# Optimization experiments

Hardware: AMD Instinct MI355X
Metric: run time of the kernel (lower is better)

Reference implementation:

```python
import jax, jax.numpy as jnp
import numpy as np

# Hard-coded module constants (from source)
E = 384      # EMBEDDING_SIZE
H = 6        # HEAD_NO
HS = 64      # HEAD_SIZE = E // H
T_CTX = 256  # CONTEXT_LENGTH
L = 6        # LAYER_NO
V = 50257    # vocab_size (init kwarg)
B = 16       # batch
T = 256      # sequence length (== context length)


def setup_inputs() -> dict:
    key = jax.random.key(0)
    ks = jax.random.split(key, 12)
    p = lambda k, shape: jax.random.normal(k, shape, dtype=jnp.float32) * 0.02
    return {
        "idx": jax.random.randint(ks[0], (B, T), 0, V),
        "tok_emb": p(ks[1], (V, E)),
        "pos_emb": p(ks[2], (T_CTX, E)),
        # per-layer stacked params; per-head q/k/v weights concatenated into [E, E]
        "Wq": p(ks[3], (L, E, E)),
        "Wk": p(ks[4], (L, E, E)),
        "Wv": p(ks[5], (L, E, E)),
        "Wo": p(ks[6], (L, E, E)),
        "bo": jnp.zeros((L, E), jnp.float32),
        "ln1_g": jnp.ones((L, E), jnp.float32),
        "ln1_b": jnp.zeros((L, E), jnp.float32),
        "ln2_g": jnp.ones((L, E), jnp.float32),
        "ln2_b": jnp.zeros((L, E), jnp.float32),
        "Wm": p(ks[7], (L, E, E)),  # MLP: single Linear(E,E) + ReLU
        "bm": jnp.zeros((L, E), jnp.float32),
        "lnf_g": jnp.ones((E,), jnp.float32),
        "lnf_b": jnp.zeros((E,), jnp.float32),
        "Wlm": p(ks[8], (E, V)),
        "blm": jnp.zeros((V,), jnp.float32),
    }


def _layernorm(x, g, b):
    mu = jnp.mean(x, axis=-1, keepdims=True)
    var = jnp.var(x, axis=-1, keepdims=True)  # biased, matches torch LayerNorm
    return (x - mu) / jnp.sqrt(var + 1e-5) * g + b


def _forward(idx, tok_emb, pos_emb, Wq, Wk, Wv, Wo, bo, ln1_g, ln1_b,
             ln2_g, ln2_b, Wm, bm, lnf_g, lnf_b, Wlm, blm):
    Bb, Tt = idx.shape
    x = tok_emb[idx] + pos_emb[:Tt]                        # [B,T,E]
    causal = jnp.tril(jnp.ones((Tt, Tt), bool))            # tril buffer
    scale = 1.0 / jnp.sqrt(jnp.float32(HS))

    def block(x, lp):
        wq, wk, wv, wo, bo_, g1, b1, g2, b2, wm, bm_ = lp
        h = _layernorm(x, g1, b1)
        q = (h @ wq).reshape(Bb, Tt, H, HS)
        k = (h @ wk).reshape(Bb, Tt, H, HS)
        v = (h @ wv).reshape(Bb, Tt, H, HS)
        s = jnp.einsum('bqhd,bkhd->bhqk', q, k)
        # source: masked_fill(-inf) then divide by sqrt(HS); -inf stays -inf
        s = jnp.where(causal, s, -jnp.inf) * scale
        a = jax.nn.softmax(s, axis=-1)                     # dropout: eval mode (no-op)
        o = jnp.einsum('bhqk,bkhd->bqhd', a, v).reshape(Bb, Tt, E)
        x = x + (o @ wo + bo_)                             # proj + residual
        h2 = _layernorm(x, g2, b2)
        x = x + jax.nn.relu(h2 @ wm + bm_)                 # MLP is Linear+ReLU only
        return x, None

    x, _ = jax.lax.scan(block, x, (Wq, Wk, Wv, Wo, bo, ln1_g, ln1_b,
                                   ln2_g, ln2_b, Wm, bm))
    x = _layernorm(x, lnf_g, lnf_b)
    return x @ Wlm + blm                                   # [B,T,V] logits


def reference(idx, tok_emb, pos_emb, Wq, Wk, Wv, Wo, bo, ln1_g, ln1_b,
              ln2_g, ln2_b, Wm, bm, lnf_g, lnf_b, Wlm, blm):
    return _forward(idx, tok_emb, pos_emb, Wq, Wk, Wv, Wo, bo, ln1_g, ln1_b,
                    ln2_g, ln2_b, Wm, bm, lnf_g, lnf_b, Wlm, blm)
```

## Files before the change

kernel.cpp:

```cpp
#include <hip/hip_runtime.h>
#include <hip/hip_bf16.h>
#include <math.h>

#define E_DIM 384
#define N_HEAD 6
#define HEAD_SZ 64
#define SEQ 256
#define BATCH 16
#define NTOK 4096
#define NLAYER 6
#define VOCAB 50257
#define VPAD 50304
#define QKV_N 1152
#define NBH 96

typedef __attribute__((ext_vector_type(8))) short bf16x8;
typedef __attribute__((ext_vector_type(4))) float f32x4;

__device__ __forceinline__ void gload16(const void* g, void* l) {
    __builtin_amdgcn_global_load_lds((const __attribute__((address_space(1))) char*)g,
                                     (__attribute__((address_space(3))) char*)l, 16, 0, 0);
}

__global__ void embed_kernel(const int* __restrict__ idx,
                             const float* __restrict__ tok,
                             const float* __restrict__ pos,
                             float* __restrict__ x) {
    int i = blockIdx.x * blockDim.x + threadIdx.x;
    if (i >= NTOK * E_DIM) return;
    int m = i / E_DIM, e = i - m * E_DIM;
    int t = m & (SEQ - 1);
    x[i] = tok[(size_t)idx[m] * E_DIM + e] + pos[t * E_DIM + e];
}

__global__ __launch_bounds__(256) void ln_kernel(const float* __restrict__ x,
                                                 const float* __restrict__ g,
                                                 const float* __restrict__ b,
                                                 __hip_bfloat16* __restrict__ h) {
    int lane = threadIdx.x & 63;
    int wave = threadIdx.x >> 6;
    int row  = blockIdx.x * 4 + wave;
    const float* xr = x + (size_t)row * E_DIM;
    float v[6];
    float s = 0.f;
#pragma unroll
    for (int c = 0; c < 6; ++c) { v[c] = xr[lane + 64 * c]; s += v[c]; }
#pragma unroll
    for (int off = 32; off > 0; off >>= 1) s += __shfl_xor(s, off);
    float mu = s * (1.0f / E_DIM);
    float s2 = 0.f;
#pragma unroll
    for (int c = 0; c < 6; ++c) { float d = v[c] - mu; s2 += d * d; }
#pragma unroll
    for (int off = 32; off > 0; off >>= 1) s2 += __shfl_xor(s2, off);
    float rstd = rsqrtf(s2 * (1.0f / E_DIM) + 1e-5f);
    __hip_bfloat16* hr = h + (size_t)row * E_DIM;
#pragma unroll
    for (int c = 0; c < 6; ++c) {
        int e = lane + 64 * c;
        hr[e] = __float2bfloat16((v[c] - mu) * rstd * g[e] + b[e]);
    }
}

__device__ __forceinline__ void tconv_tile(const float* __restrict__ src,
                                           __hip_bfloat16* __restrict__ dst,
                                           int K, int N, int n0, int k0) {
    __shared__ float tbuf[64][65];
    int c = threadIdx.x & 63, r4 = threadIdx.x >> 6;
#pragma unroll
    for (int i = 0; i < 16; ++i) {
        int r = r4 * 16 + i;
        float v = 0.f;
        if (n0 + c < N) v = src[(size_t)(k0 + r) * N + n0 + c];
        tbuf[r][c] = v;
    }
    __syncthreads();
#pragma unroll
    for (int i = 0; i < 16; ++i) {
        int rn = r4 * 16 + i;
        dst[(size_t)(n0 + rn) * K + k0 + c] = __float2bfloat16(tbuf[c][rn]);
    }
}

__global__ __launch_bounds__(256) void tconv_layers(const float* __restrict__ Wq,
                                                    const float* __restrict__ Wk,
                                                    const float* __restrict__ Wv,
                                                    const float* __restrict__ Wo,
                                                    const float* __restrict__ Wm,
                                                    __hip_bfloat16* __restrict__ WtL) {
    int z = blockIdx.z;
    int l = z / 5, t = z - l * 5;
    const float* src;
    int dstoff;
    switch (t) {
        case 0: src = Wq; dstoff = 0;    break;
        case 1: src = Wk; dstoff = 384;  break;
        case 2: src = Wv; dstoff = 768;  break;
        case 3: src = Wo; dstoff = 1152; break;
        default: src = Wm; dstoff = 1536;
    }
    src += (size_t)l * E_DIM * E_DIM;
    __hip_bfloat16* dst = WtL + ((size_t)l * 1920 + dstoff) * E_DIM;
    tconv_tile(src, dst, E_DIM, E_DIM, blockIdx.x * 64, blockIdx.y * 64);
}

__global__ __launch_bounds__(256) void tconv_lm(const float* __restrict__ Wlm,
                                                __hip_bfloat16* __restrict__ dst) {
    tconv_tile(Wlm, dst, E_DIM, VOCAB, blockIdx.x * 64, blockIdx.y * 64);
}

__global__ __launch_bounds__(256) void qkvgemm(const __hip_bfloat16* __restrict__ A,
                                               const __hip_bfloat16* __restrict__ Bt,
                                               __hip_bfloat16* __restrict__ qb,
                                               __hip_bfloat16* __restrict__ kb,
                                               __hip_bfloat16* __restrict__ vt) {
    __shared__ __align__(1024) char lds[65536];
    int tid = threadIdx.x;
    int lane = tid & 63, w = tid >> 6;
    int wm = w >> 1, wn = w & 1;
    int row0 = blockIdx.y * 128;
    int col0 = blockIdx.x * 128;

    f32x4 acc[4][4];
#pragma unroll
    for (int i = 0; i < 4; ++i)
#pragma unroll
        for (int j = 0; j < 4; ++j) acc[i][j] = (f32x4){0.f, 0.f, 0.f, 0.f};

    auto stage = [&](int buf, int k0) {
        char* Ab = lds + buf * 32768;
        char* Bb = Ab + 16384;
#pragma unroll
        for (int i = 0; i < 4; ++i) {
            int p  = i * 4096 + tid * 16;
            int lg = p ^ (((p >> 7) & 7) << 4);
            int r  = lg >> 7, cb = lg & 127;
            gload16((const char*)(A  + (size_t)(row0 + r) * E_DIM + k0) + cb, Ab + i * 4096 + w * 1024);
            gload16((const char*)(Bt + (size_t)(col0 + r) * E_DIM + k0) + cb, Bb + i * 4096 + w * 1024);
        }
    };

    stage(0, 0);
    for (int kt = 0; kt < 6; ++kt) {
        __syncthreads();
        if (kt < 5) stage((kt + 1) & 1, (kt + 1) * 64);
        const char* Ab = lds + (kt & 1) * 32768;
        const char* Bb = Ab + 16384;
#pragma unroll
        for (int ks = 0; ks < 2; ++ks) {
            bf16x8 af[4], bfr[4];
#pragma unroll
            for (int mi = 0; mi < 4; ++mi) {
                int rl = wm * 64 + mi * 16 + (lane & 15);
                int lg = rl * 128 + ks * 64 + ((lane >> 4) << 4);
                int ph = lg ^ ((rl & 7) << 4);
                af[mi] = *(const bf16x8*)(Ab + ph);
            }
#pragma unroll
            for (int ni = 0; ni < 4; ++ni) {
                int rl = wn * 64 + ni * 16 + (lane & 15);
                int lg = rl * 128 + ks * 64 + ((lane >> 4) << 4);
                int ph = lg ^ ((rl & 7) << 4);
                bfr[ni] = *(const bf16x8*)(Bb + ph);
            }
#pragma unroll
            for (int mi = 0; mi < 4; ++mi)
#pragma unroll
                for (int ni = 0; ni < 4; ++ni)
                    acc[mi][ni] = __builtin_amdgcn_mfma_f32_16x16x32_bf16(
                        af[mi], bfr[ni], acc[mi][ni], 0, 0, 0);
        }
    }

#pragma unroll
    for (int mi = 0; mi < 4; ++mi) {
#pragma unroll
        for (int ni = 0; ni < 4; ++ni) {
            int gcl = col0 + wn * 64 + ni * 16 + (lane & 15);
            int which = gcl / 384;
            int rem = gcl - which * 384;
            int h = rem >> 6, d = rem & 63;
            int gr0 = row0 + wm * 64 + mi * 16 + ((lane >> 4) << 2);
#pragma unroll
            for (int j = 0; j < 4; ++j) {
                int gr = gr0 + j;
                int b = gr >> 8, t = gr & 255;
                int bh = b * N_HEAD + h;
                __hip_bfloat16 v = __float2bfloat16(acc[mi][ni][j]);
                if (which == 0)      qb[(((size_t)bh << 8) + t) * 64 + d] = v;
                else if (which == 1) kb[(((size_t)bh << 8) + t) * 64 + d] = v;
                else                 vt[(((size_t)bh << 6) + d) * SEQ + t] = v;
            }
        }
    }
}

template <int RELU>
__global__ __launch_bounds__(256) void egemm_ln(const __hip_bfloat16* __restrict__ A,
                                                const __hip_bfloat16* __restrict__ Bt,
                                                const float* __restrict__ bias,
                                                const float* __restrict__ xin,
                                                float* __restrict__ xout,
                                                const float* __restrict__ g,
                                                const float* __restrict__ bvec,
                                                __hip_bfloat16* __restrict__ hout) {
    __shared__ __align__(1024) char lds[106496];
    float* xt = (float*)lds;
    int tid = threadIdx.x;
    int lane = tid & 63, w = tid >> 6;
    int row0 = blockIdx.x * 32;

    f32x4 acc[2][6];
#pragma unroll
    for (int i = 0; i < 2; ++i)
#pragma unroll
        for (int j = 0; j < 6; ++j) acc[i][j] = (f32x4){0.f, 0.f, 0.f, 0.f};

    auto stage = [&](int buf, int k0) {
        char* Bb = lds + buf * 53248;
        char* Ab = Bb + 49152;
        {
            int p  = tid * 16;
            int lg = p ^ (((p >> 7) & 7) << 4);
            int r  = lg >> 7, cb = lg & 127;
            gload16((const char*)(A + (size_t)(row0 + r) * E_DIM + k0) + cb, Ab + w * 1024);
        }
#pragma unroll
        for (int i = 0; i < 12; ++i) {
            int p  = i * 4096 + tid * 16;
            int lg = p ^ (((p >> 7) & 7) << 4);
            int r  = lg >> 7, cb = lg & 127;
            gload16((const char*)(Bt + (size_t)r * E_DIM + k0) + cb, Bb + i * 4096 + w * 1024);
        }
    };

    stage(0, 0);
    for (int kt = 0; kt < 6; ++kt) {
        __syncthreads();
        if (kt < 5) stage((kt + 1) & 1, (kt + 1) * 64);
        const char* Bb = lds + (kt & 1) * 53248;
        const char* Ab = Bb + 49152;
#pragma unroll
        for (int ks = 0; ks < 2; ++ks) {
            bf16x8 af[2], bfr[6];
#pragma unroll
            for (int mi = 0; mi < 2; ++mi) {
                int rl = mi * 16 + (lane & 15);
                int lg = rl * 128 + ks * 64 + ((lane >> 4) << 4);
                int ph = lg ^ ((rl & 7) << 4);
                af[mi] = *(const bf16x8*)(Ab + ph);
            }
#pragma unroll
            for (int ni = 0; ni < 6; ++ni) {
                int rl = w * 96 + ni * 16 + (lane & 15);
                int lg = rl * 128 + ks * 64 + ((lane >> 4) << 4);
                int ph = lg ^ ((rl & 7) << 4);
                bfr[ni] = *(const bf16x8*)(Bb + ph);
            }
#pragma unroll
            for (int mi = 0; mi < 2; ++mi)
#pragma unroll
                for (int ni = 0; ni < 6; ++ni)
                    acc[mi][ni] = __builtin_amdgcn_mfma_f32_16x16x32_bf16(
                        af[mi], bfr[ni], acc[mi][ni], 0, 0, 0);
        }
    }
    __syncthreads();

#pragma unroll
    for (int mi = 0; mi < 2; ++mi) {
#pragma unroll
        for (int ni = 0; ni < 6; ++ni) {
            int gc = w * 96 + ni * 16 + (lane & 15);
            int lr0 = mi * 16 + ((lane >> 4) << 2);
            float bv = bias[gc];
#pragma unroll
            for (int j = 0; j < 4; ++j) {
                int lr = lr0 + j;
                float u = acc[mi][ni][j] + bv;
                if (RELU) u = fmaxf(u, 0.f);
                float xn = xin[(size_t)(row0 + lr) * E_DIM + gc] + u;
                xout[(size_t)(row0 + lr) * E_DIM + gc] = xn;
                xt[lr * 392 + gc] = xn;
            }
        }
    }
    __syncthreads();

#pragma unroll
    for (int r8 = 0; r8 < 8; ++r8) {
        int r = w * 8 + r8;
        float v[6];
        float s = 0.f;
#pragma unroll
        for (int c = 0; c < 6; ++c) { v[c] = xt[r * 392 + lane + 64 * c]; s += v[c]; }
#pragma unroll
        for (int off = 32; off > 0; off >>= 1) s += __shfl_xor(s, off);
        float mu = s * (1.0f / E_DIM);
        float s2 = 0.f;
#pragma unroll
        for (int c = 0; c < 6; ++c) { float d = v[c] - mu; s2 += d * d; }
#pragma unroll
        for (int off = 32; off > 0; off >>= 1) s2 += __shfl_xor(s2, off);
        float rstd = rsqrtf(s2 * (1.0f / E_DIM) + 1e-5f);
        __hip_bfloat16* hr = hout + (size_t)(row0 + r) * E_DIM;
#pragma unroll
        for (int c = 0; c < 6; ++c) {
            int e = lane + 64 * c;
            hr[e] = __float2bfloat16((v[c] - mu) * rstd * g[e] + bvec[e]);
        }
    }
}

__global__ __launch_bounds__(256) void mgemm_lm(const __hip_bfloat16* __restrict__ A,
                                                const __hip_bfloat16* __restrict__ Bt,
                                                const float* __restrict__ bias,
                                                float* __restrict__ C) {
    __shared__ __align__(1024) char lds[32768];
    char* Ar = lds;
    char* Br = lds + 16384;
    int tid = threadIdx.x;
    int lane = tid & 63, w = tid >> 6;
    int wm = w >> 1, wn = w & 1;

    int wg  = blockIdx.y * 393 + blockIdx.x;
    int swz = (wg & 7) * 1572 + (wg >> 3);
    int bx  = swz % 393, by = swz / 393;
    int row0 = by * 128;
    int col0 = bx * 128;

    f32x4 acc[4][4];
#pragma unroll
    for (int i = 0; i < 4; ++i)
#pragma unroll
        for (int j = 0; j < 4; ++j) acc[i][j] = (f32x4){0.f, 0.f, 0.f, 0.f};

    for (int k0 = 0; k0 < E_DIM; k0 += 64) {
        __syncthreads();
#pragma unroll
        for (int i = 0; i < 4; ++i) {
            int p  = i * 4096 + tid * 16;
            int lg = p ^ (((p >> 7) & 7) << 4);
            int r  = lg >> 7, cb = lg & 127;
            gload16((const char*)(A  + (size_t)(row0 + r) * E_DIM + k0) + cb, Ar + i * 4096 + w * 1024);
            gload16((const char*)(Bt + (size_t)(col0 + r) * E_DIM + k0) + cb, Br + i * 4096 + w * 1024);
        }
        __syncthreads();
#pragma unroll
        for (int ks = 0; ks < 2; ++ks) {
            bf16x8 af[4], bfr[4];
#pragma unroll
            for (int mi = 0; mi < 4; ++mi) {
                int rl = wm * 64 + mi * 16 + (lane & 15);
                int lg = rl * 128 + ks * 64 + ((lane >> 4) << 4);
                int ph = lg ^ ((rl & 7) << 4);
                af[mi] = *(const bf16x8*)(Ar + ph);
            }
#pragma unroll
            for (int ni = 0; ni < 4; ++ni) {
                int rl = wn * 64 + ni * 16 + (lane & 15);
                int lg = rl * 128 + ks * 64 + ((lane >> 4) << 4);
                int ph = lg ^ ((rl & 7) << 4);
                bfr[ni] = *(const bf16x8*)(Br + ph);
            }
#pragma unroll
            for (int mi = 0; mi < 4; ++mi)
#pragma unroll
                for (int ni = 0; ni < 4; ++ni)
                    acc[mi][ni] = __builtin_amdgcn_mfma_f32_16x16x32_bf16(
                        af[mi], bfr[ni], acc[mi][ni], 0, 0, 0);
        }
    }

#pragma unroll
    for (int mi = 0; mi < 4; ++mi) {
#pragma unroll
        for (int ni = 0; ni < 4; ++ni) {
            int gr = row0 + wm * 64 + mi * 16 + ((lane >> 4) << 2);
            int gc = col0 + wn * 64 + ni * 16 + (lane & 15);
            if (gc < VOCAB) {
                float bv = bias[gc];
#pragma unroll
                for (int j = 0; j < 4; ++j)
                    C[(size_t)(gr + j) * VOCAB + gc] = acc[mi][ni][j] + bv;
            }
        }
    }
}

#define ATT_K 0
#define ATT_V 32768
#define ATT_Q 65536

__global__ __launch_bounds__(256) void attn_fused(const __hip_bfloat16* __restrict__ qb,
                                                  const __hip_bfloat16* __restrict__ kb,
                                                  const __hip_bfloat16* __restrict__ vt,
                                                  __hip_bfloat16* __restrict__ o) {
    __shared__ __align__(1024) char lds[73728];
    int tid = threadIdx.x;
    int lane = tid & 63, w = tid >> 6;
    int bh = blockIdx.x;
    int mq = blockIdx.y;
    int b = bh / N_HEAD, h = bh - b * N_HEAD;

    const char* kg = (const char*)(kb + (size_t)bh * SEQ * 64);
#pragma unroll
    for (int i = 0; i < 8; ++i) {
        int p = i * 4096 + tid * 16;
        int lg = p ^ (((p >> 7) & 7) << 4);
        gload16(kg + lg, lds + ATT_K + p);
    }
    const char* vg = (const char*)(vt + (size_t)bh * 64 * SEQ);
#pragma unroll
    for (int i = 0; i < 8; ++i) {
        int p = i * 4096 + tid * 16;
        int lg = p ^ (((p >> 9) & 7) << 4);
        gload16(vg + lg, lds + ATT_V + p);
    }
    const char* qg = (const char*)(qb + ((size_t)bh * SEQ + mq * 64) * 64);
#pragma unroll
    for (int i = 0; i < 2; ++i) {
        int p = i * 4096 + tid * 16;
        int lg = p ^ (((p >> 7) & 7) << 4);
        gload16(qg + lg, lds + ATT_Q + p);
    }
    __syncthreads();

    int q0 = w * 16;
    int qg0 = mq * 64 + q0;

    f32x4 acc[16];
#pragma unroll
    for (int n = 0; n < 16; ++n) acc[n] = (f32x4){0.f, 0.f, 0.f, 0.f};
#pragma unroll
    for (int ks = 0; ks < 2; ++ks) {
        int rq = q0 + (lane & 15);
        int byq = (ks * 64 + ((lane >> 4) << 4)) ^ ((rq & 7) << 4);
        bf16x8 aq = *(const bf16x8*)(lds + ATT_Q + rq * 128 + byq);
#pragma unroll
        for (int n = 0; n < 16; ++n) {
            int rk = n * 16 + (lane & 15);
            int byk = (ks * 64 + ((lane >> 4) << 4)) ^ ((rk & 7) << 4);
            bf16x8 bk = *(const bf16x8*)(lds + ATT_K + rk * 128 + byk);
            acc[n] = __builtin_amdgcn_mfma_f32_16x16x32_bf16(aq, bk, acc[n], 0, 0, 0);
        }
    }
    __syncthreads();

    char* pbase = lds + ATT_K + w * 8192;
#pragma unroll
    for (int j = 0; j < 4; ++j) {
        int rql = ((lane >> 4) << 2) + j;
        int rg = qg0 + rql;
        float s[16];
        float m = -INFINITY;
#pragma unroll
        for (int n = 0; n < 16; ++n) {
            int cg = n * 16 + (lane & 15);
            float v = (cg <= rg) ? acc[n][j] * 0.125f : -INFINITY;
            s[n] = v;
            m = fmaxf(m, v);
        }
#pragma unroll
        for (int off = 1; off < 16; off <<= 1) m = fmaxf(m, __shfl_xor(m, off));
        float sum = 0.f;
#pragma unroll
        for (int n = 0; n < 16; ++n) { s[n] = __expf(s[n] - m); sum += s[n]; }
#pragma unroll
        for (int off = 1; off < 16; off <<= 1) sum += __shfl_xor(sum, off);
        float inv = 1.0f / sum;
#pragma unroll
        for (int n = 0; n < 16; ++n) {
            int cg = n * 16 + (lane & 15);
            int by = (cg * 2) ^ ((rql & 7) << 4);
            *(__hip_bfloat16*)(pbase + rql * 512 + by) = __float2bfloat16(s[n] * inv);
        }
    }

    f32x4 oacc[4];
#pragma unroll
    for (int nf = 0; nf < 4; ++nf) oacc[nf] = (f32x4){0.f, 0.f, 0.f, 0.f};
#pragma unroll
    for (int ks = 0; ks < 8; ++ks) {
        int rp = lane & 15;
        int byp = (ks * 64 + ((lane >> 4) << 4)) ^ ((rp & 7) << 4);
        bf16x8 ap = *(const bf16x8*)(pbase + rp * 512 + byp);
#pragma unroll
        for (int nf = 0; nf < 4; ++nf) {
            int rv = nf * 16 + (lane & 15);
            int byv = (ks * 64 + ((lane >> 4) << 4)) ^ ((rv & 7) << 4);
            bf16x8 bv = *(const bf16x8*)(lds + ATT_V + rv * 512 + byv);
            oacc[nf] = __builtin_amdgcn_mfma_f32_16x16x32_bf16(ap, bv, oacc[nf], 0, 0, 0);
        }
    }

#pragma unroll
    for (int nf = 0; nf < 4; ++nf) {
#pragma unroll
        for (int j = 0; j < 4; ++j) {
            int t = mq * 64 + q0 + ((lane >> 4) << 2) + j;
            int d = nf * 16 + (lane & 15);
            o[(size_t)(b * SEQ + t) * E_DIM + h * 64 + d] = __float2bfloat16(oacc[nf][j]);
        }
    }
}

extern "C" void kernel_launch(void* const* d_in, const int* in_sizes, int n_in,
                              void* d_out, int out_size, void* d_ws, size_t ws_size,
                              hipStream_t stream) {
    const int*   idx  = (const int*)d_in[0];
    const float* tok  = (const float*)d_in[1];
    const float* pos  = (const float*)d_in[2];
    const float* Wq   = (const float*)d_in[3];
    const float* Wk   = (const float*)d_in[4];
    const float* Wv   = (const float*)d_in[5];
    const float* Wo   = (const float*)d_in[6];
    const float* bo   = (const float*)d_in[7];
    const float* ln1g = (const float*)d_in[8];
    const float* ln1b = (const float*)d_in[9];
    const float* ln2g = (const float*)d_in[10];
    const float* ln2b = (const float*)d_in[11];
    const float* Wm   = (const float*)d_in[12];
    const float* bm   = (const float*)d_in[13];
    const float* lnfg = (const float*)d_in[14];
    const float* lnfb = (const float*)d_in[15];
    const float* Wlm  = (const float*)d_in[16];
    const float* blm  = (const float*)d_in[17];
    float* out = (float*)d_out;

    float*           x    = (float*)d_ws;
    __hip_bfloat16*  hb   = (__hip_bfloat16*)(x + (size_t)NTOK * E_DIM);
    __hip_bfloat16*  WtL  = hb + (size_t)NTOK * E_DIM;
    __hip_bfloat16*  WtLM = WtL + (size_t)NLAYER * 1920 * E_DIM;
    __hip_bfloat16*  qbv  = WtLM + (size_t)VPAD * E_DIM;
    __hip_bfloat16*  kbv  = qbv + (size_t)NBH * SEQ * 64;
    __hip_bfloat16*  vtb  = kbv + (size_t)NBH * SEQ * 64;

    embed_kernel<<<(NTOK * E_DIM + 255) / 256, 256, 0, stream>>>(idx, tok, pos, x);
    tconv_layers<<<dim3(6, 6, NLAYER * 5), 256, 0, stream>>>(Wq, Wk, Wv, Wo, Wm, WtL);
    tconv_lm<<<dim3(VPAD / 64, E_DIM / 64), 256, 0, stream>>>(Wlm, WtLM);
    ln_kernel<<<NTOK / 4, 256, 0, stream>>>(x, ln1g, ln1b, hb);

    for (int l = 0; l < NLAYER; ++l) {
        const __hip_bfloat16* wl = WtL + (size_t)l * 1920 * E_DIM;
        qkvgemm<<<dim3(QKV_N / 128, NTOK / 128), 256, 0, stream>>>(hb, wl, qbv, kbv, vtb);
        attn_fused<<<dim3(NBH, 4), 256, 0, stream>>>(qbv, kbv, vtb, hb);
        egemm_ln<0><<<NTOK / 32, 256, 0, stream>>>(hb, wl + (size_t)1152 * E_DIM,
                                                   bo + l * E_DIM, x, x,
                                                   ln2g + l * E_DIM, ln2b + l * E_DIM, hb);
        const float* ng = (l == NLAYER - 1) ? lnfg : ln1g + (l + 1) * E_DIM;
        const float* nb = (l == NLAYER - 1) ? lnfb : ln1b + (l + 1) * E_DIM;
        egemm_ln<1><<<NTOK / 32, 256, 0, stream>>>(hb, wl + (size_t)1536 * E_DIM,
                                                   bm + l * E_DIM, x, x,
                                                   ng, nb, hb);
    }

    mgemm_lm<<<dim3(VPAD / 128, NTOK / 128), 256, 0, stream>>>(hb, WtLM, blm, out);
}
```

Baseline: 754.7 us.

## Double-buffer LDS in LM-head GEMM to overlap global loads with MFMA

Turns the LM-head GEMM K loop into a two-stage software pipeline. The next K-tile is loaded into a second LDS buffer with global_load_lds while the current tile is computed, using explicit vmcnt waits and barriers, and the loop is fully unrolled. This is meant to hide global-memory latency behind the MFMA work. LDS per block doubles to 64KB, which may lower the number of resident blocks per CU.

```diff
diff --git a/kernel.cpp b/kernel.cpp
--- a/kernel.cpp
+++ b/kernel.cpp
@@ -316,9 +316,7 @@
                                                 const __hip_bfloat16* __restrict__ Bt,
                                                 const float* __restrict__ bias,
                                                 float* __restrict__ C) {
-    __shared__ __align__(1024) char lds[32768];
-    char* Ar = lds;
-    char* Br = lds + 16384;
+    __shared__ __align__(1024) char lds[65536];
     int tid = threadIdx.x;
     int lane = tid & 63, w = tid >> 6;
     int wm = w >> 1, wn = w & 1;
@@ -335,17 +333,22 @@
 #pragma unroll
         for (int j = 0; j < 4; ++j) acc[i][j] = (f32x4){0.f, 0.f, 0.f, 0.f};
 
-    for (int k0 = 0; k0 < E_DIM; k0 += 64) {
-        __syncthreads();
+    auto stage = [&](int buf, int k0) {
+        char* Ab = lds + buf * 32768;
+        char* Bb = Ab + 16384;
 #pragma unroll
         for (int i = 0; i < 4; ++i) {
             int p  = i * 4096 + tid * 16;
             int lg = p ^ (((p >> 7) & 7) << 4);
             int r  = lg >> 7, cb = lg & 127;
-            gload16((const char*)(A  + (size_t)(row0 + r) * E_DIM + k0) + cb, Ar + i * 4096 + w * 1024);
-            gload16((const char*)(Bt + (size_t)(col0 + r) * E_DIM + k0) + cb, Br + i * 4096 + w * 1024);
-        }
-        __syncthreads();
+            gload16((const char*)(A  + (size_t)(row0 + r) * E_DIM + k0) + cb, Ab + i * 4096 + w * 1024);
+            gload16((const char*)(Bt + (size_t)(col0 + r) * E_DIM + k0) + cb, Bb + i * 4096 + w * 1024);
+        }
+    };
+
+    auto compute = [&](int buf) {
+        const char* Ab = lds + buf * 32768;
+        const char* Bb = Ab + 16384;
 #pragma unroll
         for (int ks = 0; ks < 2; ++ks) {
             bf16x8 af[4], bfr[4];
@@ -354,14 +357,14 @@
                 int rl = wm * 64 + mi * 16 + (lane & 15);
                 int lg = rl * 128 + ks * 64 + ((lane >> 4) << 4);
                 int ph = lg ^ ((rl & 7) << 4);
-                af[mi] = *(const bf16x8*)(Ar + ph);
+                af[mi] = *(const bf16x8*)(Ab + ph);
             }
 #pragma unroll
             for (int ni = 0; ni < 4; ++ni) {
                 int rl = wn * 64 + ni * 16 + (lane & 15);
                 int lg = rl * 128 + ks * 64 + ((lane >> 4) << 4);
                 int ph = lg ^ ((rl & 7) << 4);
-                bfr[ni] = *(const bf16x8*)(Br + ph);
+                bfr[ni] = *(const bf16x8*)(Bb + ph);
             }
 #pragma unroll
             for (int mi = 0; mi < 4; ++mi)
@@ -370,7 +373,30 @@
                     acc[mi][ni] = __builtin_amdgcn_mfma_f32_16x16x32_bf16(
                         af[mi], bfr[ni], acc[mi][ni], 0, 0, 0);
         }
-    }
+    };
+
+    stage(0, 0);
+    stage(1, 64);
+
+#define LM_ITER(T, VM)                                                  \
+    asm volatile("s_waitcnt vmcnt(" #VM ")" ::: "memory");              \
+    __builtin_amdgcn_sched_barrier(0);                                  \
+    __builtin_amdgcn_s_barrier();                                       \
+    __builtin_amdgcn_sched_barrier(0);                                  \
+    compute(T & 1);                                                     \
+    asm volatile("s_waitcnt lgkmcnt(0)" ::: "memory");                  \
+    __builtin_amdgcn_sched_barrier(0);                                  \
+    __builtin_amdgcn_s_barrier();                                       \
+    __builtin_amdgcn_sched_barrier(0);                                  \
+    if ((T) + 2 < 6) stage((T) & 1, ((T) + 2) * 64);
+
+    LM_ITER(0, 8)
+    LM_ITER(1, 8)
+    LM_ITER(2, 8)
+    LM_ITER(3, 8)
+    LM_ITER(4, 8)
+    LM_ITER(5, 0)
+#undef LM_ITER
 
 #pragma unroll
     for (int mi = 0; mi < 4; ++mi) {
```

Result: no change. 759.2 us (+0.6%).

## Fuse out-proj and MLP GEMMs into one tail kernel; merge embed+LN and weight converts

Applied to the files above, without the earlier changes.

Merges the attention output projection, residual, LN2, MLP GEMM with ReLU, residual and the next LN into a single kernel. The LN2 output stays in swizzled LDS instead of round-tripping through global memory, and the residual is kept in registers. The embedding gather is fused with the first LayerNorm, and the two weight-transpose kernels are merged into one launch. This cuts launches and global traffic, but the fused kernel uses 128KB of LDS per block, which limits occupancy to one block per CU.

```diff
diff --git a/kernel.cpp b/kernel.cpp
--- a/kernel.cpp
+++ b/kernel.cpp
@@ -22,29 +22,34 @@
                                      (__attribute__((address_space(3))) char*)l, 16, 0, 0);
 }
 
-__global__ void embed_kernel(const int* __restrict__ idx,
-                             const float* __restrict__ tok,
-                             const float* __restrict__ pos,
-                             float* __restrict__ x) {
-    int i = blockIdx.x * blockDim.x + threadIdx.x;
-    if (i >= NTOK * E_DIM) return;
-    int m = i / E_DIM, e = i - m * E_DIM;
-    int t = m & (SEQ - 1);
-    x[i] = tok[(size_t)idx[m] * E_DIM + e] + pos[t * E_DIM + e];
-}
-
-__global__ __launch_bounds__(256) void ln_kernel(const float* __restrict__ x,
-                                                 const float* __restrict__ g,
-                                                 const float* __restrict__ b,
-                                                 __hip_bfloat16* __restrict__ h) {
+__device__ __forceinline__ unsigned short bfbits(float x) {
+    __hip_bfloat16 h = __float2bfloat16(x);
+    return *reinterpret_cast<unsigned short*>(&h);
+}
+
+__global__ __launch_bounds__(256) void emln(const int* __restrict__ idx,
+                                            const float* __restrict__ tok,
+                                            const float* __restrict__ pos,
+                                            const float* __restrict__ g,
+                                            const float* __restrict__ b,
+                                            float* __restrict__ x,
+                                            __hip_bfloat16* __restrict__ h) {
     int lane = threadIdx.x & 63;
-    int wave = threadIdx.x >> 6;
-    int row  = blockIdx.x * 4 + wave;
-    const float* xr = x + (size_t)row * E_DIM;
+    int w = threadIdx.x >> 6;
+    int row = blockIdx.x * 4 + w;
+    int t = row & (SEQ - 1);
+    const float* tr = tok + (size_t)idx[row] * E_DIM;
+    const float* pr = pos + (size_t)t * E_DIM;
+    float* xr = x + (size_t)row * E_DIM;
     float v[6];
     float s = 0.f;
 #pragma unroll
-    for (int c = 0; c < 6; ++c) { v[c] = xr[lane + 64 * c]; s += v[c]; }
+    for (int c = 0; c < 6; ++c) {
+        int e = lane + 64 * c;
+        v[c] = tr[e] + pr[e];
+        xr[e] = v[c];
+        s += v[c];
+    }
 #pragma unroll
     for (int off = 32; off > 0; off >>= 1) s += __shfl_xor(s, off);
     float mu = s * (1.0f / E_DIM);
@@ -82,31 +87,36 @@
     }
 }
 
-__global__ __launch_bounds__(256) void tconv_layers(const float* __restrict__ Wq,
-                                                    const float* __restrict__ Wk,
-                                                    const float* __restrict__ Wv,
-                                                    const float* __restrict__ Wo,
-                                                    const float* __restrict__ Wm,
-                                                    __hip_bfloat16* __restrict__ WtL) {
-    int z = blockIdx.z;
-    int l = z / 5, t = z - l * 5;
-    const float* src;
-    int dstoff;
-    switch (t) {
-        case 0: src = Wq; dstoff = 0;    break;
-        case 1: src = Wk; dstoff = 384;  break;
-        case 2: src = Wv; dstoff = 768;  break;
-        case 3: src = Wo; dstoff = 1152; break;
-        default: src = Wm; dstoff = 1536;
-    }
-    src += (size_t)l * E_DIM * E_DIM;
-    __hip_bfloat16* dst = WtL + ((size_t)l * 1920 + dstoff) * E_DIM;
-    tconv_tile(src, dst, E_DIM, E_DIM, blockIdx.x * 64, blockIdx.y * 64);
-}
-
-__global__ __launch_bounds__(256) void tconv_lm(const float* __restrict__ Wlm,
-                                                __hip_bfloat16* __restrict__ dst) {
-    tconv_tile(Wlm, dst, E_DIM, VOCAB, blockIdx.x * 64, blockIdx.y * 64);
+__global__ __launch_bounds__(256) void tconv_all(const float* __restrict__ Wq,
+                                                 const float* __restrict__ Wk,
+                                                 const float* __restrict__ Wv,
+                                                 const float* __restrict__ Wo,
+                                                 const float* __restrict__ Wm,
+                                                 const float* __restrict__ Wlm,
+                                                 __hip_bfloat16* __restrict__ WtL,
+                                                 __hip_bfloat16* __restrict__ WtLM) {
+    int bid = blockIdx.x;
+    if (bid < 1080) {
+        int z = bid / 36, rem = bid - z * 36;
+        int bx = rem % 6, by = rem / 6;
+        int l = z / 5, t = z - l * 5;
+        const float* src;
+        int dstoff;
+        switch (t) {
+            case 0: src = Wq; dstoff = 0;    break;
+            case 1: src = Wk; dstoff = 384;  break;
+            case 2: src = Wv; dstoff = 768;  break;
+            case 3: src = Wo; dstoff = 1152; break;
+            default: src = Wm; dstoff = 1536;
+        }
+        src += (size_t)l * E_DIM * E_DIM;
+        __hip_bfloat16* dst = WtL + ((size_t)l * 1920 + dstoff) * E_DIM;
+        tconv_tile(src, dst, E_DIM, E_DIM, bx * 64, by * 64);
+    } else {
+        int b2 = bid - 1080;
+        int bx = b2 % 786, by = b2 / 786;
+        tconv_tile(Wlm, WtLM, E_DIM, VOCAB, bx * 64, by * 64);
+    }
 }
 
 __global__ __launch_bounds__(256) void qkvgemm(const __hip_bfloat16* __restrict__ A,
@@ -195,36 +205,47 @@
     }
 }
 
-template <int RELU>
-__global__ __launch_bounds__(256) void egemm_ln(const __hip_bfloat16* __restrict__ A,
-                                                const __hip_bfloat16* __restrict__ Bt,
-                                                const float* __restrict__ bias,
-                                                const float* __restrict__ xin,
-                                                float* __restrict__ xout,
-                                                const float* __restrict__ g,
-                                                const float* __restrict__ bvec,
-                                                __hip_bfloat16* __restrict__ hout) {
-    __shared__ __align__(1024) char lds[106496];
-    float* xt = (float*)lds;
+__global__ __launch_bounds__(256) void tail_fused(const __hip_bfloat16* __restrict__ A,
+                                                  const __hip_bfloat16* __restrict__ WoT,
+                                                  const float* __restrict__ bo,
+                                                  const __hip_bfloat16* __restrict__ WmT,
+                                                  const float* __restrict__ bm,
+                                                  const float* __restrict__ xin,
+                                                  float* __restrict__ xout,
+                                                  const float* __restrict__ g2,
+                                                  const float* __restrict__ b2v,
+                                                  const float* __restrict__ gn,
+                                                  const float* __restrict__ bnv,
+                                                  __hip_bfloat16* __restrict__ hout) {
+    __shared__ __align__(1024) char lds[131072];
+    char* Bbuf = lds;
+    char* Abuf = lds + 98304;
+    float* xt  = (float*)(lds + 49152);
+    char* h2   = lds + 106496;
     int tid = threadIdx.x;
     int lane = tid & 63, w = tid >> 6;
     int row0 = blockIdx.x * 32;
 
+    float xnew[2][6][4];
+#pragma unroll
+    for (int mi = 0; mi < 2; ++mi)
+#pragma unroll
+        for (int ni = 0; ni < 6; ++ni) {
+            int gc = w * 96 + ni * 16 + (lane & 15);
+            int lr0 = mi * 16 + ((lane >> 4) << 2);
+#pragma unroll
+            for (int j = 0; j < 4; ++j)
+                xnew[mi][ni][j] = xin[(size_t)(row0 + lr0 + j) * E_DIM + gc];
+        }
+
     f32x4 acc[2][6];
 #pragma unroll
     for (int i = 0; i < 2; ++i)
 #pragma unroll
         for (int j = 0; j < 6; ++j) acc[i][j] = (f32x4){0.f, 0.f, 0.f, 0.f};
 
-    auto stage = [&](int buf, int k0) {
-        char* Bb = lds + buf * 53248;
-        char* Ab = Bb + 49152;
-        {
-            int p  = tid * 16;
-            int lg = p ^ (((p >> 7) & 7) << 4);
-            int r  = lg >> 7, cb = lg & 127;
-            gload16((const char*)(A + (size_t)(row0 + r) * E_DIM + k0) + cb, Ab + w * 1024);
-        }
+    auto stageB = [&](const __hip_bfloat16* Bt, int buf, int k0) {
+        char* Bb = Bbuf + buf * 49152;
 #pragma unroll
         for (int i = 0; i < 12; ++i) {
             int p  = i * 4096 + tid * 16;
@@ -233,13 +254,21 @@
             gload16((const char*)(Bt + (size_t)r * E_DIM + k0) + cb, Bb + i * 4096 + w * 1024);
         }
     };
-
-    stage(0, 0);
+    auto stageA = [&](int buf, int k0) {
+        int p  = tid * 16;
+        int lg = p ^ (((p >> 7) & 7) << 4);
+        int r  = lg >> 7, cb = lg & 127;
+        gload16((const char*)(A + (size_t)(row0 + r) * E_DIM + k0) + cb,
+                Abuf + buf * 4096 + w * 1024);
+    };
+
+    stageA(0, 0);
+    stageB(WoT, 0, 0);
     for (int kt = 0; kt < 6; ++kt) {
         __syncthreads();
-        if (kt < 5) stage((kt + 1) & 1, (kt + 1) * 64);
-        const char* Bb = lds + (kt & 1) * 53248;
-        const char* Ab = Bb + 49152;
+        if (kt < 5) { stageA((kt + 1) & 1, (kt + 1) * 64); stageB(WoT, (kt + 1) & 1, (kt + 1) * 64); }
+        const char* Ab = Abuf + (kt & 1) * 4096;
+        const char* Bb = Bbuf + (kt & 1) * 49152;
 #pragma unroll
         for (int ks = 0; ks < 2; ++ks) {
             bf16x8 af[2], bfr[6];
@@ -266,6 +295,7 @@
         }
     }
     __syncthreads();
+    stageB(WmT, 0, 0);
 
 #pragma unroll
     for (int mi = 0; mi < 2; ++mi) {
@@ -273,15 +303,12 @@
         for (int ni = 0; ni < 6; ++ni) {
             int gc = w * 96 + ni * 16 + (lane & 15);
             int lr0 = mi * 16 + ((lane >> 4) << 2);
-            float bv = bias[gc];
+            float bv = bo[gc];
 #pragma unroll
             for (int j = 0; j < 4; ++j) {
-                int lr = lr0 + j;
-                float u = acc[mi][ni][j] + bv;
-                if (RELU) u = fmaxf(u, 0.f);
-                float xn = xin[(size_t)(row0 + lr) * E_DIM + gc] + u;
-                xout[(size_t)(row0 + lr) * E_DIM + gc] = xn;
-                xt[lr * 392 + gc] = xn;
+                float xn = xnew[mi][ni][j] + acc[mi][ni][j] + bv;
+                xnew[mi][ni][j] = xn;
+                xt[(lr0 + j) * 392 + gc] = xn;
             }
         }
     }
@@ -303,11 +330,90 @@
 #pragma unroll
         for (int off = 32; off > 0; off >>= 1) s2 += __shfl_xor(s2, off);
         float rstd = rsqrtf(s2 * (1.0f / E_DIM) + 1e-5f);
-        __hip_bfloat16* hr = hout + (size_t)(row0 + r) * E_DIM;
 #pragma unroll
         for (int c = 0; c < 6; ++c) {
             int e = lane + 64 * c;
-            hr[e] = __float2bfloat16((v[c] - mu) * rstd * g[e] + bvec[e]);
+            unsigned short u = bfbits((v[c] - mu) * rstd * g2[e] + b2v[e]);
+            int by = (2 * e) ^ ((r & 7) << 4);
+            *(unsigned short*)(h2 + r * 768 + by) = u;
+        }
+    }
+
+#pragma unroll
+    for (int i = 0; i < 2; ++i)
+#pragma unroll
+        for (int j = 0; j < 6; ++j) acc[i][j] = (f32x4){0.f, 0.f, 0.f, 0.f};
+
+    for (int kt = 0; kt < 6; ++kt) {
+        __syncthreads();
+        if (kt < 5) stageB(WmT, (kt + 1) & 1, (kt + 1) * 64);
+        const char* Bb = Bbuf + (kt & 1) * 49152;
+#pragma unroll
+        for (int ks = 0; ks < 2; ++ks) {
+            bf16x8 af[2], bfr[6];
+#pragma unroll
+            for (int mi = 0; mi < 2; ++mi) {
+                int rl = mi * 16 + (lane & 15);
+                int koff = kt * 128 + ks * 64 + ((lane >> 4) << 4);
+                int by = koff ^ ((rl & 7) << 4);
+                af[mi] = *(const bf16x8*)(h2 + rl * 768 + by);
+            }
+#pragma unroll
+            for (int ni = 0; ni < 6; ++ni) {
+                int rl = w * 96 + ni * 16 + (lane & 15);
+                int lg = rl * 128 + ks * 64 + ((lane >> 4) << 4);
+                int ph = lg ^ ((rl & 7) << 4);
+                bfr[ni] = *(const bf16x8*)(Bb + ph);
+            }
+#pragma unroll
+            for (int mi = 0; mi < 2; ++mi)
+#pragma unroll
+                for (int ni = 0; ni < 6; ++ni)
+                    acc[mi][ni] = __builtin_amdgcn_mfma_f32_16x16x32_bf16(
+                        af[mi], bfr[ni], acc[mi][ni], 0, 0, 0);
+        }
+    }
+    __syncthreads();
+
+#pragma unroll
+    for (int mi = 0; mi < 2; ++mi) {
+#pragma unroll
+        for (int ni = 0; ni < 6; ++ni) {
+            int gc = w * 96 + ni * 16 + (lane & 15);
+            int lr0 = mi * 16 + ((lane >> 4) << 2);
+            float bv = bm[gc];
+#pragma unroll
+            for (int j = 0; j < 4; ++j) {
+                float u = fmaxf(acc[mi][ni][j] + bv, 0.f);
+                float xn = xnew[mi][ni][j] + u;
+                xout[(size_t)(row0 + lr0 + j) * E_DIM + gc] = xn;
+                xt[(lr0 + j) * 392 + gc] = xn;
+            }
+        }
+    }
+    __syncthreads();
+
+#pragma unroll
+    for (int r8 = 0; r8 < 8; ++r8) {
+        int r = w * 8 + r8;
+        float v[6];
+        float s = 0.f;
+#pragma unroll
+        for (int c = 0; c < 6; ++c) { v[c] = xt[r * 392 + lane + 64 * c]; s += v[c]; }
+#pragma unroll
+        for (int off = 32; off > 0; off >>= 1) s += __shfl_xor(s, off);
+        float mu = s * (1.0f / E_DIM);
+        float s2 = 0.f;
+#pragma unroll
+        for (int c = 0; c < 6; ++c) { float d = v[c] - mu; s2 += d * d; }
+#pragma unroll
+        for (int off = 32; off > 0; off >>= 1) s2 += __shfl_xor(s2, off);
+        float rstd = rsqrtf(s2 * (1.0f / E_DIM) + 1e-5f);
+        __hip_bfloat16* hr = hout + (size_t)(row0 + r) * E_DIM;
+#pragma unroll
+        for (int c = 0; c < 6; ++c) {
+            int e = lane + 64 * c;
+            hr[e] = __float2bfloat16((v[c] - mu) * rstd * gn[e] + bnv[e]);
         }
     }
 }
@@ -536,23 +642,22 @@
     __hip_bfloat16*  kbv  = qbv + (size_t)NBH * SEQ * 64;
     __hip_bfloat16*  vtb  = kbv + (size_t)NBH * SEQ * 64;
 
-    embed_kernel<<<(NTOK * E_DIM + 255) / 256, 256, 0, stream>>>(idx, tok, pos, x);
-    tconv_layers<<<dim3(6, 6, NLAYER * 5), 256, 0, stream>>>(Wq, Wk, Wv, Wo, Wm, WtL);
-    tconv_lm<<<dim3(VPAD / 64, E_DIM / 64), 256, 0, stream>>>(Wlm, WtLM);
-    ln_kernel<<<NTOK / 4, 256, 0, stream>>>(x, ln1g, ln1b, hb);
+    emln<<<NTOK / 4, 256, 0, stream>>>(idx, tok, pos, ln1g, ln1b, x, hb);
+    tconv_all<<<1080 + 786 * 6, 256, 0, stream>>>(Wq, Wk, Wv, Wo, Wm, Wlm, WtL, WtLM);
 
     for (int l = 0; l < NLAYER; ++l) {
         const __hip_bfloat16* wl = WtL + (size_t)l * 1920 * E_DIM;
         qkvgemm<<<dim3(QKV_N / 128, NTOK / 128), 256, 0, stream>>>(hb, wl, qbv, kbv, vtb);
         attn_fused<<<dim3(NBH, 4), 256, 0, stream>>>(qbv, kbv, vtb, hb);
-        egemm_ln<0><<<NTOK / 32, 256, 0, stream>>>(hb, wl + (size_t)1152 * E_DIM,
-                                                   bo + l * E_DIM, x, x,
-                                                   ln2g + l * E_DIM, ln2b + l * E_DIM, hb);
         const float* ng = (l == NLAYER - 1) ? lnfg : ln1g + (l + 1) * E_DIM;
         const float* nb = (l == NLAYER - 1) ? lnfb : ln1b + (l + 1) * E_DIM;
-        egemm_ln<1><<<NTOK / 32, 256, 0, stream>>>(hb, wl + (size_t)1536 * E_DIM,
-                                                   bm + l * E_DIM, x, x,
-                                                   ng, nb, hb);
+        tail_fused<<<NTOK / 32, 256, 0, stream>>>(hb, wl + (size_t)1152 * E_DIM,
+                                                  bo + l * E_DIM,
+                                                  wl + (size_t)1536 * E_DIM,
+                                                  bm + l * E_DIM,
+                                                  x, x,
+                                                  ln2g + l * E_DIM, ln2b + l * E_DIM,
+                                                  ng, nb, hb);
     }
 
     mgemm_lm<<<dim3(VPAD / 128, NTOK / 128), 256, 0, stream>>>(hb, WtLM, blm, out);
```

Measured after the change: 728.8 us. -3.4%, faster.
